# Performance work log

Measured on AMD Instinct MI355X. Metric: run time of the kernel, lower is better.

The kernel has to match this reference:

```python
import jax, jax.numpy as jnp
import numpy as np

B, L, EMB, H, NL, E, MAXA, PAD = 64, 512, 400, 256, 3, 512, 32, 0


def setup_inputs() -> dict:
    key = jax.random.key(0)
    ks = jax.random.split(key, 12)
    s = lambda k, shape: jax.random.normal(k, shape, jnp.float32) * 0.02
    Semb = jax.random.normal(ks[0], (B, EMB, L), jnp.float32)
    word_ids = jax.random.randint(ks[1], (B, L), 0, 30000)
    y1 = jax.random.randint(ks[2], (B,), 0, L - MAXA)
    span = jax.random.randint(ks[3], (B,), 0, MAXA)
    y2 = y1 + span
    edges = jax.random.randint(ks[4], (B, E, 2), 0, L)
    return dict(
        Semb=Semb,
        ans_sent_word_ids=word_ids,
        y1_in_sent=y1,
        y2_in_sent=y2,
        edges=edges,
        W1=s(ks[5], (H, EMB)),                 # Initialized_Conv1d (k=1, no bias)
        hw_lin_W=s(ks[6], (2, H, H)), hw_lin_b=jnp.zeros((2, H), jnp.float32),
        hw_gate_W=s(ks[7], (2, H, H)), hw_gate_b=jnp.zeros((2, H), jnp.float32),
        gcn_W=s(ks[8], (NL, H, H)), gcn_b=jnp.zeros((NL, H), jnp.float32),
        conv_W=s(ks[9], (1, NL * H)), conv_b=jnp.zeros((1,), jnp.float32),
        lin_W=s(ks[10], (L, L)), lin_b=jnp.zeros((L,), jnp.float32),
    )


def reference(Semb, ans_sent_word_ids, y1_in_sent, y2_in_sent, edges,
              W1, hw_lin_W, hw_lin_b, hw_gate_W, hw_gate_b,
              gcn_W, gcn_b, conv_W, conv_b, lin_W, lin_b):
    # 1x1 conv: [B, EMB, L] -> [B, H, L]
    x = jnp.einsum('oi,bit->bot', W1, Semb)
    # 2-layer Highway (dropout is identity in eval)
    for i in range(2):
        gate = jax.nn.sigmoid(jnp.einsum('oi,bit->bot', hw_gate_W[i], x) + hw_gate_b[i][None, :, None])
        nonlin = jnp.einsum('oi,bit->bot', hw_lin_W[i], x) + hw_lin_b[i][None, :, None]
        x = gate * nonlin + (1.0 - gate) * x
    maskS = (ans_sent_word_ids != PAD).astype(x.dtype)            # [B, L]
    # answer-span mask (Aemb itself is dead code in the original forward's output)
    pos = y1_in_sent[:, None] + jnp.arange(MAXA)                   # [B, MAXA]
    maskA = (pos <= y2_in_sent[:, None]).astype(x.dtype)
    # dense adjacency from edge list (undirected since gcn_directed=False)
    bidx = jnp.broadcast_to(jnp.arange(B)[:, None], (B, E))
    adj = jnp.zeros((B, L, L), x.dtype)
    adj = adj.at[bidx, edges[..., 0], edges[..., 1]].set(1.0)
    adj = adj.at[bidx, edges[..., 1], edges[..., 0]].set(1.0)
    # GCN (C-GCN style: W(Ax) + W(x), note bias counted twice, /(deg+1), relu)
    h = x.transpose(0, 2, 1)                                       # [B, L, H]
    denom = jnp.sum(adj, axis=2, keepdims=True) + 1.0              # [B, L, 1]
    outs = []
    for l in range(NL):
        Ax = jnp.einsum('bls,bsh->blh', adj, h)
        AxW = jnp.einsum('blh,oh->blo', Ax + h, gcn_W[l]) + 2.0 * gcn_b[l]
        h = jax.nn.relu(AxW / denom)
        outs.append(h)
    cat = jnp.concatenate(outs, axis=2)                            # [B, L, NL*H]
    y = jax.nn.relu(jnp.einsum('blc,oc->bol', cat, conv_W) + conv_b[None, :, None])  # [B,1,L]
    logits = (jnp.einsum('bol,ml->bom', y, lin_W) + lin_b).squeeze(1)                # [B,L]
    logits = logits * maskS + (1.0 - maskS) * (-1e30)
    return (logits, maskA)
```

## Files before the change

### kernel.cpp

```cpp
#include <hip/hip_runtime.h>
#include <cstdint>

#define B 64
#define L 512
#define EMB 400
#define KPAD 448
#define H 256
#define NL 3
#define NE 512
#define MAXA 32
#define M_TOT (B * L)

typedef unsigned short u16;
typedef float f32x4 __attribute__((ext_vector_type(4)));
typedef short short8 __attribute__((ext_vector_type(8)));
typedef u16 u16x8 __attribute__((ext_vector_type(8)));

__device__ __forceinline__ float b2f(u16 u) {
  unsigned v = ((unsigned)u) << 16;
  return __builtin_bit_cast(float, v);
}
__device__ __forceinline__ u16 f2b(float f) {
  unsigned u = __builtin_bit_cast(unsigned, f);
  unsigned r = (u + 0x7fffu + ((u >> 16) & 1u)) >> 16;
  return (u16)r;
}

#define GL16(g, l)                                                              \
  __builtin_amdgcn_global_load_lds((const __attribute__((address_space(1))) void*)(g), \
                                   (__attribute__((address_space(3))) void*)(l), 16, 0, 0)

template <int EPI>
__global__ __launch_bounds__(256, 2) void gemm64(
    const u16* __restrict__ A, const u16* __restrict__ Bw, const u16* __restrict__ B2w,
    const int K,
    const float* __restrict__ bias1, const float* __restrict__ bias2,
    const float* __restrict__ rden, const float* __restrict__ cw,
    float* __restrict__ yv, u16* __restrict__ Out) {
  constexpr bool HW = (EPI == 1);
  __shared__ u16 Bl0[256 * 32];
  __shared__ u16 Bl1[256 * 32];
  __shared__ u16 Al0[64 * 32];
  __shared__ u16 Al1[64 * 32];
  __shared__ u16 Cl0[HW ? 256 * 32 : 8];
  __shared__ u16 Cl1[HW ? 256 * 32 : 8];

  const int t = threadIdx.x;
  const int wid = t >> 6, lane = t & 63;
  const int m0 = blockIdx.x * 64;
  const int fr = lane & 15, kg = lane >> 4;
  const int r4 = t >> 2, ksg = t & 3;

  f32x4 acc[4][4] = {};
  f32x4 acc2[4][4] = {};

  auto stage = [&](u16* Ab, u16* Bb, u16* Cb, int kk) {
    const int kc = kk * 32 + ksg * 8;
#pragma unroll
    for (int c = 0; c < 4; ++c)
      GL16(Bw + (size_t)(c * 64 + r4) * K + kc, Bb + (size_t)(c * 256 + wid * 64) * 8);
    if constexpr (HW) {
#pragma unroll
      for (int c = 0; c < 4; ++c)
        GL16(B2w + (size_t)(c * 64 + r4) * K + kc, Cb + (size_t)(c * 256 + wid * 64) * 8);
    }
    GL16(A + (size_t)(m0 + r4) * K + kc, Ab + (size_t)(wid * 64) * 8);
  };
  auto compute = [&](const u16* Ab, const u16* Bb, const u16* Cb) {
    short8 af[4], bf[4], cf[4];
#pragma unroll
    for (int i = 0; i < 4; ++i) {
      af[i] = *(const short8*)(Ab + ((size_t)(i * 16 + fr) * 4 + kg) * 8);
      bf[i] = *(const short8*)(Bb + ((size_t)(wid * 64 + i * 16 + fr) * 4 + kg) * 8);
      if constexpr (HW)
        cf[i] = *(const short8*)(Cb + ((size_t)(wid * 64 + i * 16 + fr) * 4 + kg) * 8);
    }
#pragma unroll
    for (int mi = 0; mi < 4; ++mi)
#pragma unroll
      for (int ni = 0; ni < 4; ++ni) {
        acc[mi][ni] = __builtin_amdgcn_mfma_f32_16x16x32_bf16(af[mi], bf[ni], acc[mi][ni], 0, 0, 0);
        if constexpr (HW)
          acc2[mi][ni] =
              __builtin_amdgcn_mfma_f32_16x16x32_bf16(af[mi], cf[ni], acc2[mi][ni], 0, 0, 0);
      }
  };

  const int nk = K >> 5;
  stage(Al0, Bl0, Cl0, 0);
  __syncthreads();
  for (int kk = 0; kk < nk; kk += 2) {
    if (kk + 1 < nk) stage(Al1, Bl1, Cl1, kk + 1);
    compute(Al0, Bl0, Cl0);
    __syncthreads();
    if (kk + 2 < nk) stage(Al0, Bl0, Cl0, kk + 2);
    compute(Al1, Bl1, Cl1);
    __syncthreads();
  }

  const int r0 = kg * 4;
  const int c0 = wid * 64 + fr;
  if constexpr (EPI == 0) {
#pragma unroll
    for (int ni = 0; ni < 4; ++ni) {
      const int col = c0 + ni * 16;
#pragma unroll
      for (int mi = 0; mi < 4; ++mi)
#pragma unroll
        for (int rr = 0; rr < 4; ++rr)
          Out[(size_t)(m0 + mi * 16 + r0 + rr) * H + col] = f2b(acc[mi][ni][rr]);
    }
  } else if constexpr (EPI == 1) {
#pragma unroll
    for (int ni = 0; ni < 4; ++ni) {
      const int col = c0 + ni * 16;
      const float b1 = bias1[col], b2 = bias2[col];
#pragma unroll
      for (int mi = 0; mi < 4; ++mi)
#pragma unroll
        for (int rr = 0; rr < 4; ++rr) {
          const int row = m0 + mi * 16 + r0 + rr;
          const float g = 1.f / (1.f + __expf(-(acc[mi][ni][rr] + b1)));
          const float nn = acc2[mi][ni][rr] + b2;
          const float x = b2f(A[(size_t)row * K + col]);
          Out[(size_t)row * H + col] = f2b(g * nn + (1.f - g) * x);
        }
    }
  } else {
    float ypart[16];
#pragma unroll
    for (int q = 0; q < 16; ++q) ypart[q] = 0.f;
#pragma unroll
    for (int ni = 0; ni < 4; ++ni) {
      const int col = c0 + ni * 16;
      const float b1 = 2.f * bias1[col];
      const float cwv = cw[col];
#pragma unroll
      for (int mi = 0; mi < 4; ++mi)
#pragma unroll
        for (int rr = 0; rr < 4; ++rr) {
          const int row = m0 + mi * 16 + r0 + rr;
          const float s = (acc[mi][ni][rr] + b1) * rden[row];
          const float rl = s > 0.f ? s : 0.f;
          ypart[mi * 4 + rr] += rl * cwv;
          if constexpr (EPI == 2) Out[(size_t)row * H + col] = f2b(rl);
        }
    }
#pragma unroll
    for (int q = 0; q < 16; ++q) {
      float p = ypart[q];
      p += __shfl_xor(p, 1);
      p += __shfl_xor(p, 2);
      p += __shfl_xor(p, 4);
      p += __shfl_xor(p, 8);
      if (fr == 0) atomicAdd(&yv[m0 + (q >> 2) * 16 + r0 + (q & 3)], p);
    }
  }
}

__global__ __launch_bounds__(256) void k_gather(const unsigned* __restrict__ bm,
                                                const u16* __restrict__ h,
                                                u16* __restrict__ T) {
  const int t = threadIdx.x;
  const int tok = blockIdx.x * 8 + (t >> 5);
  const int b = tok >> 9;
  const int c = (t & 31) * 8;
  const uint4* wp4 = (const uint4*)(bm + (size_t)tok * 16);
  const uint4 w0 = wp4[0], w1 = wp4[1], w2 = wp4[2], w3 = wp4[3];
  const unsigned wa[16] = {w0.x, w0.y, w0.z, w0.w, w1.x, w1.y, w1.z, w1.w,
                           w2.x, w2.y, w2.z, w2.w, w3.x, w3.y, w3.z, w3.w};
  float acc[8];
  {
    const u16x8 v = *(const u16x8*)(h + (size_t)tok * H + c);
#pragma unroll
    for (int i = 0; i < 8; ++i) acc[i] = b2f(v[i]);
  }
#pragma unroll
  for (int wi = 0; wi < 16; ++wi) {
    unsigned bits = wa[wi];
    while (bits) {
      const int bit = __ffs(bits) - 1;
      bits &= bits - 1;
      const int s = wi * 32 + bit;
      const u16x8 u = *(const u16x8*)(h + (size_t)(b * L + s) * H + c);
#pragma unroll
      for (int i = 0; i < 8; ++i) acc[i] += b2f(u[i]);
    }
  }
  u16x8 o;
#pragma unroll
  for (int i = 0; i < 8; ++i) o[i] = f2b(acc[i]);
  *(u16x8*)(T + (size_t)tok * H + c) = o;
}

__global__ __launch_bounds__(256) void k_sembT(const float* __restrict__ Semb,
                                               u16* __restrict__ A0) {
  const int b = blockIdx.x, e0 = blockIdx.y * 64, l0 = blockIdx.z * 64;
  __shared__ u16 tile[64][72];
  const int t = threadIdx.x;
  {
    const int er = t >> 2, ls = (t & 3) * 16;
    if (e0 + er < EMB) {
      const float* src = Semb + ((size_t)b * EMB + e0 + er) * L + l0 + ls;
#pragma unroll
      for (int i = 0; i < 4; ++i) {
        const float4 v = *(const float4*)(src + i * 4);
        tile[er][ls + i * 4 + 0] = f2b(v.x);
        tile[er][ls + i * 4 + 1] = f2b(v.y);
        tile[er][ls + i * 4 + 2] = f2b(v.z);
        tile[er][ls + i * 4 + 3] = f2b(v.w);
      }
    } else {
#pragma unroll
      for (int i = 0; i < 16; ++i) tile[er][ls + i] = 0;
    }
  }
  __syncthreads();
  {
    const int lr = t >> 2, es = (t & 3) * 16;
    u16x8 v0, v1;
#pragma unroll
    for (int i = 0; i < 8; ++i) v0[i] = tile[es + i][lr];
#pragma unroll
    for (int i = 0; i < 8; ++i) v1[i] = tile[es + 8 + i][lr];
    u16* dst = A0 + (size_t)(b * L + l0 + lr) * KPAD + e0 + es;
    *(u16x8*)dst = v0;
    *(u16x8*)(dst + 8) = v1;
  }
}

__global__ void k_cvtall(const float* __restrict__ W1, const float* __restrict__ gW,
                         const float* __restrict__ lW, const float* __restrict__ gcnW,
                         const unsigned* __restrict__ bm,
                         u16* __restrict__ W1b, u16* __restrict__ HWGb,
                         u16* __restrict__ HWLb, u16* __restrict__ GCNb,
                         float* __restrict__ rden) {
  int i = blockIdx.x * 256 + threadIdx.x;
  if (i < 256 * KPAD) {
    const int o = i / KPAD, k = i - o * KPAD;
    W1b[i] = (k < EMB) ? f2b(W1[o * EMB + k]) : (u16)0;
    return;
  }
  i -= 256 * KPAD;
  if (i < 2 * H * H) { HWGb[i] = f2b(gW[i]); return; }
  i -= 2 * H * H;
  if (i < 2 * H * H) { HWLb[i] = f2b(lW[i]); return; }
  i -= 2 * H * H;
  if (i < NL * H * H) { GCNb[i] = f2b(gcnW[i]); return; }
  i -= NL * H * H;
  if (i < M_TOT) {
    const uint4* p = (const uint4*)(bm + (size_t)i * 16);
    int c = 0;
#pragma unroll
    for (int w = 0; w < 4; ++w) {
      const uint4 v = p[w];
      c += __popc(v.x) + __popc(v.y) + __popc(v.z) + __popc(v.w);
    }
    rden[i] = 1.f / (1.f + (float)c);
  }
}

__global__ void k_edges(const int* __restrict__ edges, unsigned* __restrict__ bm) {
  const int t = blockIdx.x * 256 + threadIdx.x;
  const int b = t >> 9, e = t & 511;
  const int u = edges[(size_t)(b * NE + e) * 2 + 0];
  const int v = edges[(size_t)(b * NE + e) * 2 + 1];
  atomicOr(&bm[(size_t)(b * L + u) * 16 + (v >> 5)], 1u << (v & 31));
  atomicOr(&bm[(size_t)(b * L + v) * 16 + (u >> 5)], 1u << (u & 31));
}

__global__ __launch_bounds__(256) void k_logits(const float* __restrict__ yv,
                                                const float* __restrict__ cb,
                                                const float* __restrict__ lw,
                                                const float* __restrict__ lb,
                                                const int* __restrict__ wids,
                                                const int* __restrict__ y1,
                                                const int* __restrict__ y2,
                                                float* __restrict__ out) {
  if (blockIdx.x == B * 2) {
#pragma unroll
    for (int j = 0; j < 8; ++j) {
      const int idx = j * 256 + threadIdx.x;
      const int b = idx >> 5, q = idx & 31;
      out[B * L + idx] = (y1[b] + q <= y2[b]) ? 1.0f : 0.0f;
    }
    return;
  }
  const int b = blockIdx.x >> 1;
  const int m = ((blockIdx.x & 1) << 8) + threadIdx.x;
  __shared__ float ys[512];
  const float cb0 = cb[0];
  ys[threadIdx.x] = fmaxf(yv[(size_t)b * L + threadIdx.x] + cb0, 0.f);
  ys[threadIdx.x + 256] = fmaxf(yv[(size_t)b * L + 256 + threadIdx.x] + cb0, 0.f);
  __syncthreads();
  float acc = lb[m];
  const float4* wr = (const float4*)(lw + (size_t)m * L);
#pragma unroll 4
  for (int l4 = 0; l4 < 128; ++l4) {
    const float4 w4 = wr[l4];
    acc += ys[l4 * 4] * w4.x + ys[l4 * 4 + 1] * w4.y + ys[l4 * 4 + 2] * w4.z +
           ys[l4 * 4 + 3] * w4.w;
  }
  out[(size_t)b * L + m] = (wids[(size_t)b * L + m] != 0) ? acc : -1.0e30f;
}

extern "C" void kernel_launch(void* const* d_in, const int* in_sizes, int n_in,
                              void* d_out, int out_size, void* d_ws, size_t ws_size,
                              hipStream_t stream) {
  (void)in_sizes; (void)n_in; (void)out_size; (void)ws_size;
  const float* Semb      = (const float*)d_in[0];
  const int*   wids      = (const int*)d_in[1];
  const int*   y1        = (const int*)d_in[2];
  const int*   y2        = (const int*)d_in[3];
  const int*   edges     = (const int*)d_in[4];
  const float* W1        = (const float*)d_in[5];
  const float* hw_lin_W  = (const float*)d_in[6];
  const float* hw_lin_b  = (const float*)d_in[7];
  const float* hw_gate_W = (const float*)d_in[8];
  const float* hw_gate_b = (const float*)d_in[9];
  const float* gcn_W     = (const float*)d_in[10];
  const float* gcn_b     = (const float*)d_in[11];
  const float* conv_W    = (const float*)d_in[12];
  const float* conv_b    = (const float*)d_in[13];
  const float* lin_W     = (const float*)d_in[14];
  const float* lin_b     = (const float*)d_in[15];
  float* out = (float*)d_out;

  char* ws = (char*)d_ws;
  const size_t SZA = (size_t)M_TOT * KPAD * 2;
  const size_t SZX = (size_t)M_TOT * H * 2;
  u16* A0   = (u16*)(ws);
  u16* P0b  = (u16*)(ws + SZA);
  u16* P1b  = (u16*)(ws + SZA + SZX);
  u16* O0   = (u16*)(ws + SZA + 2 * SZX);
  u16* O1   = (u16*)(ws + SZA + 3 * SZX);
  char* wp  = ws + SZA + 4 * SZX;
  u16* W1b  = (u16*)(wp);
  u16* HWGb = (u16*)(wp + 229376);
  u16* HWLb = (u16*)(wp + 229376 + 262144);
  u16* GCNb = (u16*)(wp + 229376 + 2 * 262144);
  char* sp  = wp + 229376 + 2 * 262144 + 393216;
  unsigned* bm   = (unsigned*)(sp);
  float*    yv   = (float*)(sp + 2097152);
  float*    rden = (float*)(sp + 2097152 + 131072);

  hipMemsetAsync(bm, 0, 2097152 + 131072, stream);
  k_edges<<<dim3(B * NE / 256), 256, 0, stream>>>(edges, bm);

  const int ncvt = 256 * KPAD + 4 * H * H + NL * H * H + M_TOT;
  k_cvtall<<<dim3((ncvt + 255) / 256), 256, 0, stream>>>(W1, hw_gate_W, hw_lin_W, gcn_W, bm,
                                                         W1b, HWGb, HWLb, GCNb, rden);
  k_sembT<<<dim3(B, KPAD / 64, 8), 256, 0, stream>>>(Semb, A0);

  gemm64<0><<<dim3(M_TOT / 64), 256, 0, stream>>>(A0, W1b, nullptr, KPAD, nullptr, nullptr,
                                                  nullptr, nullptr, nullptr, P0b);
  gemm64<1><<<dim3(M_TOT / 64), 256, 0, stream>>>(P0b, HWGb, HWLb, H, hw_gate_b, hw_lin_b,
                                                  nullptr, nullptr, nullptr, P1b);
  gemm64<1><<<dim3(M_TOT / 64), 256, 0, stream>>>(P1b, HWGb + H * H, HWLb + H * H, H,
                                                  hw_gate_b + H, hw_lin_b + H, nullptr, nullptr,
                                                  nullptr, P0b);
  k_gather<<<dim3(M_TOT / 8), 256, 0, stream>>>(bm, P0b, P1b);
  gemm64<2><<<dim3(M_TOT / 64), 256, 0, stream>>>(P1b, GCNb, nullptr, H, gcn_b, nullptr,
                                                  rden, conv_W, yv, O0);
  k_gather<<<dim3(M_TOT / 8), 256, 0, stream>>>(bm, O0, P0b);
  gemm64<2><<<dim3(M_TOT / 64), 256, 0, stream>>>(P0b, GCNb + H * H, nullptr, H, gcn_b + H,
                                                  nullptr, rden, conv_W + H, yv, O1);
  k_gather<<<dim3(M_TOT / 8), 256, 0, stream>>>(bm, O1, P1b);
  gemm64<3><<<dim3(M_TOT / 64), 256, 0, stream>>>(P1b, GCNb + 2 * H * H, nullptr, H,
                                                  gcn_b + 2 * H, nullptr, rden,
                                                  conv_W + 2 * H, yv, nullptr);

  k_logits<<<dim3(B * 2 + 1), 256, 0, stream>>>(yv, conv_b, lin_W, lin_b, wids, y1, y2, out);
}
```

Measured before the change: 181.2 us.

## Pipeline GEMM loads with vmcnt waits, shrink K padding, merge prep kernels

Rewrites the GEMM main loop as a single-stage ping-pong. The next tile's global loads are issued before computing the current tile, and partial s_waitcnt vmcnt with raw s_barrier replaces full __syncthreads, so loads stay in flight across compute. It also cuts the padded EMB dimension from 448 to 416 to skip K work, and fuses the transpose and weight-conversion kernels into one launch. The hand-written vmcnt counts depend on the exact number of loads issued per stage, which is fragile if the compiler reorders or splits loads.

```diff
diff --git a/kernel.cpp b/kernel.cpp
--- a/kernel.cpp
+++ b/kernel.cpp
@@ -4,7 +4,7 @@
 #define B 64
 #define L 512
 #define EMB 400
-#define KPAD 448
+#define KPAD 416
 #define H 256
 #define NL 3
 #define NE 512
@@ -88,14 +88,27 @@
 
   const int nk = K >> 5;
   stage(Al0, Bl0, Cl0, 0);
-  __syncthreads();
-  for (int kk = 0; kk < nk; kk += 2) {
-    if (kk + 1 < nk) stage(Al1, Bl1, Cl1, kk + 1);
-    compute(Al0, Bl0, Cl0);
-    __syncthreads();
-    if (kk + 2 < nk) stage(Al0, Bl0, Cl0, kk + 2);
-    compute(Al1, Bl1, Cl1);
-    __syncthreads();
+  for (int kk = 0; kk < nk; ++kk) {
+    u16* Ac = (kk & 1) ? Al1 : Al0;
+    u16* Bc = (kk & 1) ? Bl1 : Bl0;
+    u16* Cc = (kk & 1) ? Cl1 : Cl0;
+    u16* An = (kk & 1) ? Al0 : Al1;
+    u16* Bn = (kk & 1) ? Bl0 : Bl1;
+    u16* Cn = (kk & 1) ? Cl0 : Cl1;
+    if (kk + 1 < nk) {
+      stage(An, Bn, Cn, kk + 1);
+      if constexpr (HW)
+        asm volatile("s_waitcnt vmcnt(9)" ::: "memory");
+      else
+        asm volatile("s_waitcnt vmcnt(5)" ::: "memory");
+    } else {
+      asm volatile("s_waitcnt vmcnt(0)" ::: "memory");
+    }
+    __builtin_amdgcn_s_barrier();
+    asm volatile("" ::: "memory");
+    compute(Ac, Bc, Cc);
+    __builtin_amdgcn_s_barrier();
+    asm volatile("" ::: "memory");
   }
 
   const int r0 = kg * 4;
@@ -193,49 +206,66 @@
   *(u16x8*)(T + (size_t)tok * H + c) = o;
 }
 
-__global__ __launch_bounds__(256) void k_sembT(const float* __restrict__ Semb,
-                                               u16* __restrict__ A0) {
-  const int b = blockIdx.x, e0 = blockIdx.y * 64, l0 = blockIdx.z * 64;
-  __shared__ u16 tile[64][72];
+__global__ void k_edges(const int* __restrict__ edges, unsigned* __restrict__ bm) {
+  const int t = blockIdx.x * 256 + threadIdx.x;
+  const int b = t >> 9, e = t & 511;
+  const int u = edges[(size_t)(b * NE + e) * 2 + 0];
+  const int v = edges[(size_t)(b * NE + e) * 2 + 1];
+  atomicOr(&bm[(size_t)(b * L + u) * 16 + (v >> 5)], 1u << (v & 31));
+  atomicOr(&bm[(size_t)(b * L + v) * 16 + (u >> 5)], 1u << (u & 31));
+}
+
+#define NSEMBT (B * 56)
+__global__ __launch_bounds__(256) void k_prep(const float* __restrict__ Semb,
+                                              const float* __restrict__ W1,
+                                              const float* __restrict__ gW,
+                                              const float* __restrict__ lW,
+                                              const float* __restrict__ gcnW,
+                                              const unsigned* __restrict__ bm,
+                                              u16* __restrict__ A0,
+                                              u16* __restrict__ W1b, u16* __restrict__ HWGb,
+                                              u16* __restrict__ HWLb, u16* __restrict__ GCNb,
+                                              float* __restrict__ rden) {
   const int t = threadIdx.x;
-  {
-    const int er = t >> 2, ls = (t & 3) * 16;
-    if (e0 + er < EMB) {
-      const float* src = Semb + ((size_t)b * EMB + e0 + er) * L + l0 + ls;
-#pragma unroll
-      for (int i = 0; i < 4; ++i) {
-        const float4 v = *(const float4*)(src + i * 4);
-        tile[er][ls + i * 4 + 0] = f2b(v.x);
-        tile[er][ls + i * 4 + 1] = f2b(v.y);
-        tile[er][ls + i * 4 + 2] = f2b(v.z);
-        tile[er][ls + i * 4 + 3] = f2b(v.w);
+  if (blockIdx.x < NSEMBT) {
+    const int bid = blockIdx.x;
+    const int b = bid / 56, rem = bid - b * 56;
+    const int e0 = (rem >> 3) * 64, l0 = (rem & 7) * 64;
+    __shared__ u16 tile[64][72];
+    {
+      const int er = t >> 2, ls = (t & 3) * 16;
+      if (e0 + er < EMB) {
+        const float* src = Semb + ((size_t)b * EMB + e0 + er) * L + l0 + ls;
+#pragma unroll
+        for (int i = 0; i < 4; ++i) {
+          const float4 v = *(const float4*)(src + i * 4);
+          tile[er][ls + i * 4 + 0] = f2b(v.x);
+          tile[er][ls + i * 4 + 1] = f2b(v.y);
+          tile[er][ls + i * 4 + 2] = f2b(v.z);
+          tile[er][ls + i * 4 + 3] = f2b(v.w);
+        }
+      } else {
+#pragma unroll
+        for (int i = 0; i < 16; ++i) tile[er][ls + i] = 0;
       }
-    } else {
-#pragma unroll
-      for (int i = 0; i < 16; ++i) tile[er][ls + i] = 0;
-    }
-  }
-  __syncthreads();
-  {
-    const int lr = t >> 2, es = (t & 3) * 16;
-    u16x8 v0, v1;
-#pragma unroll
-    for (int i = 0; i < 8; ++i) v0[i] = tile[es + i][lr];
-#pragma unroll
-    for (int i = 0; i < 8; ++i) v1[i] = tile[es + 8 + i][lr];
-    u16* dst = A0 + (size_t)(b * L + l0 + lr) * KPAD + e0 + es;
-    *(u16x8*)dst = v0;
-    *(u16x8*)(dst + 8) = v1;
-  }
-}
-
-__global__ void k_cvtall(const float* __restrict__ W1, const float* __restrict__ gW,
-                         const float* __restrict__ lW, const float* __restrict__ gcnW,
-                         const unsigned* __restrict__ bm,
-                         u16* __restrict__ W1b, u16* __restrict__ HWGb,
-                         u16* __restrict__ HWLb, u16* __restrict__ GCNb,
-                         float* __restrict__ rden) {
-  int i = blockIdx.x * 256 + threadIdx.x;
+    }
+    __syncthreads();
+    {
+      const int lr = t >> 2, es = (t & 3) * 16;
+      if (e0 + es < KPAD) {
+        u16x8 v0, v1;
+#pragma unroll
+        for (int i = 0; i < 8; ++i) v0[i] = tile[es + i][lr];
+#pragma unroll
+        for (int i = 0; i < 8; ++i) v1[i] = tile[es + 8 + i][lr];
+        u16* dst = A0 + (size_t)(b * L + l0 + lr) * KPAD + e0 + es;
+        *(u16x8*)dst = v0;
+        *(u16x8*)(dst + 8) = v1;
+      }
+    }
+    return;
+  }
+  int i = (blockIdx.x - NSEMBT) * 256 + t;
   if (i < 256 * KPAD) {
     const int o = i / KPAD, k = i - o * KPAD;
     W1b[i] = (k < EMB) ? f2b(W1[o * EMB + k]) : (u16)0;
@@ -258,15 +288,6 @@
     }
     rden[i] = 1.f / (1.f + (float)c);
   }
-}
-
-__global__ void k_edges(const int* __restrict__ edges, unsigned* __restrict__ bm) {
-  const int t = blockIdx.x * 256 + threadIdx.x;
-  const int b = t >> 9, e = t & 511;
-  const int u = edges[(size_t)(b * NE + e) * 2 + 0];
-  const int v = edges[(size_t)(b * NE + e) * 2 + 1];
-  atomicOr(&bm[(size_t)(b * L + u) * 16 + (v >> 5)], 1u << (v & 31));
-  atomicOr(&bm[(size_t)(b * L + v) * 16 + (u >> 5)], 1u << (u & 31));
 }
 
 __global__ __launch_bounds__(256) void k_logits(const float* __restrict__ yv,
@@ -336,10 +357,10 @@
   u16* O1   = (u16*)(ws + SZA + 3 * SZX);
   char* wp  = ws + SZA + 4 * SZX;
   u16* W1b  = (u16*)(wp);
-  u16* HWGb = (u16*)(wp + 229376);
-  u16* HWLb = (u16*)(wp + 229376 + 262144);
-  u16* GCNb = (u16*)(wp + 229376 + 2 * 262144);
-  char* sp  = wp + 229376 + 2 * 262144 + 393216;
+  u16* HWGb = (u16*)(wp + 212992);
+  u16* HWLb = (u16*)(wp + 212992 + 262144);
+  u16* GCNb = (u16*)(wp + 212992 + 2 * 262144);
+  char* sp  = wp + 212992 + 2 * 262144 + 393216;
   unsigned* bm   = (unsigned*)(sp);
   float*    yv   = (float*)(sp + 2097152);
   float*    rden = (float*)(sp + 2097152 + 131072);
@@ -348,9 +369,8 @@
   k_edges<<<dim3(B * NE / 256), 256, 0, stream>>>(edges, bm);
 
   const int ncvt = 256 * KPAD + 4 * H * H + NL * H * H + M_TOT;
-  k_cvtall<<<dim3((ncvt + 255) / 256), 256, 0, stream>>>(W1, hw_gate_W, hw_lin_W, gcn_W, bm,
-                                                         W1b, HWGb, HWLb, GCNb, rden);
-  k_sembT<<<dim3(B, KPAD / 64, 8), 256, 0, stream>>>(Semb, A0);
+  k_prep<<<dim3(NSEMBT + (ncvt + 255) / 256), 256, 0, stream>>>(
+      Semb, W1, hw_gate_W, hw_lin_W, gcn_W, bm, A0, W1b, HWGb, HWLb, GCNb, rden);
 
   gemm64<0><<<dim3(M_TOT / 64), 256, 0, stream>>>(A0, W1b, nullptr, KPAD, nullptr, nullptr,
                                                   nullptr, nullptr, nullptr, P0b);
```

After: 181.3 us. About the same (+0.0%).
